# Optimization experiments

Hardware: AMD Instinct MI355X
Metric: run time of the kernel (lower is better)

Reference implementation:

```python
import jax, jax.numpy as jnp
import numpy as np
import math

DIM = 1024
DIM_HEAD = 64
HEADS = 16
HIDDEN = DIM_HEAD * HEADS
EPS = 1e-5


def layer_norm(x, g, b):
    m = jnp.mean(x, axis=-1, keepdims=True)
    v = jnp.var(x, axis=-1, keepdims=True)
    return (x - m) * jax.lax.rsqrt(v + EPS) * g + b


def setup_inputs() -> dict:
    key = jax.random.key(0)
    ks = jax.random.split(key, 8)
    B, n, n_l = 8, 4096, 64
    x = jax.random.normal(ks[0], (B, n, DIM), dtype=jnp.float32)
    latents = jax.random.normal(ks[1], (B, n_l, DIM), dtype=jnp.float32)
    # LayerNorm params
    g_media = jnp.ones((DIM,), jnp.float32)
    b_media = jnp.zeros((DIM,), jnp.float32)
    g_lat = jnp.ones((DIM,), jnp.float32)
    b_lat = jnp.zeros((DIM,), jnp.float32)
    # Linear weights stored as [in, out] so y = x @ W (no bias, as in source)
    s = 1.0 / math.sqrt(DIM)
    Wq = jax.random.uniform(ks[2], (DIM, HIDDEN), jnp.float32, -s, s)
    Wkv = jax.random.uniform(ks[3], (DIM, 2 * HIDDEN), jnp.float32, -s, s)
    so = 1.0 / math.sqrt(HIDDEN)
    Wout = jax.random.uniform(ks[4], (HIDDEN, DIM), jnp.float32, -so, so)
    return {"x": x, "latents": latents, "g_media": g_media, "b_media": b_media,
            "g_lat": g_lat, "b_lat": b_lat, "Wq": Wq, "Wkv": Wkv, "Wout": Wout}


def reference(x, latents, g_media, b_media, g_lat, b_lat, Wq, Wkv, Wout):
    B, n, _ = x.shape
    n_l = latents.shape[1]
    scale = math.sqrt(DIM_HEAD)

    xn = layer_norm(x, g_media, b_media)          # [B, n, D]
    ln_ = layer_norm(latents, g_lat, b_lat)       # [B, n_l, D]

    ctx = jnp.concatenate([xn, ln_], axis=1)      # [B, n+n_l, D]

    q = (ln_ @ Wq).reshape(B, n_l, HEADS, DIM_HEAD).transpose(0, 2, 1, 3)
    kv = ctx @ Wkv                                 # [B, n+n_l, 2*HIDDEN]
    k, v = jnp.split(kv, 2, axis=-1)
    k = k.reshape(B, n + n_l, HEADS, DIM_HEAD).transpose(0, 2, 1, 3)
    v = v.reshape(B, n + n_l, HEADS, DIM_HEAD).transpose(0, 2, 1, 3)

    # scores: [B, H, n_l, n+n_l]; note: no pre-softmax scaling (faithful to source)
    scores = jnp.einsum('bhqd,bhkd->bhqk', q, k)
    scores = scores - jax.lax.stop_gradient(jnp.max(scores, axis=-1, keepdims=True))
    attn = jax.nn.softmax(scores, axis=-1) / scale  # post-softmax scale (faithful)

    out = jnp.einsum('bhqk,bhkd->bhqd', attn, v)   # [B, H, n_l, d]
    out = out.transpose(0, 2, 1, 3).reshape(B, n_l, HIDDEN)
    return out @ Wout                               # [B, n_l, D]
```

## Files before the change

kernel.cpp:

```cpp
#include <hip/hip_runtime.h>

typedef unsigned short u16;
typedef unsigned int u32;
typedef __attribute__((ext_vector_type(8))) short bf16x8;
typedef __attribute__((ext_vector_type(4))) float f32x4;

#define BB   8
#define SN   4096
#define NLQ  64
#define SS   4160
#define DD   1024
#define HH   16
#define DHD  64
#define KV2  2048
#define BNL  512

__device__ __forceinline__ u16 f2bf(float f){
  unsigned int u = __float_as_uint(f);
  u = (u + 0x7fffu + ((u >> 16) & 1u)) >> 16;
  return (u16)u;
}

__device__ __forceinline__ void stc(float* p, float v){ *p = v; }
__device__ __forceinline__ void stc(u16* p, float v){ *p = f2bf(v); }

__device__ __forceinline__ void async_copy16(const u16* g, u16* l){
  __builtin_amdgcn_global_load_lds(
      (const __attribute__((address_space(1))) unsigned int*)g,
      (__attribute__((address_space(3))) unsigned int*)l,
      16, 0, 0);
}

__global__ __launch_bounds__(256) void ln_kernel(
    const float* __restrict__ x, const float* __restrict__ lat,
    const float* __restrict__ g_m, const float* __restrict__ b_m,
    const float* __restrict__ g_l, const float* __restrict__ b_l,
    u16* __restrict__ ctx, u16* __restrict__ latn)
{
  int r = blockIdx.x;
  int b = r / SS, p = r % SS;
  bool isl = (p >= SN);
  const float* src = isl ? lat + ((size_t)b*NLQ + (p-SN))*DD
                         : x   + ((size_t)b*SN + p)*DD;
  const float* gg = isl ? g_l : g_m;
  const float* bb = isl ? b_l : b_m;
  int t = threadIdx.x;
  float4 v = ((const float4*)src)[t];
  float s = v.x + v.y + v.z + v.w;
  float q = v.x*v.x + v.y*v.y + v.z*v.z + v.w*v.w;
  #pragma unroll
  for (int off = 32; off > 0; off >>= 1){
    s += __shfl_down(s, off);
    q += __shfl_down(q, off);
  }
  __shared__ float red[12];
  int lane = t & 63, wid = t >> 6;
  if (lane == 0){ red[wid] = s; red[4+wid] = q; }
  __syncthreads();
  if (t == 0){
    float ts = red[0]+red[1]+red[2]+red[3];
    float tq = red[4]+red[5]+red[6]+red[7];
    float mean = ts * (1.0f/DD);
    float var  = tq * (1.0f/DD) - mean*mean;
    red[8] = mean;
    red[9] = rsqrtf(var + 1e-5f);
  }
  __syncthreads();
  float mean = red[8], rs = red[9];
  float4 gv = ((const float4*)gg)[t];
  float4 bv = ((const float4*)bb)[t];
  ushort4 o;
  o.x = f2bf((v.x-mean)*rs*gv.x + bv.x);
  o.y = f2bf((v.y-mean)*rs*gv.y + bv.y);
  o.z = f2bf((v.z-mean)*rs*gv.z + bv.z);
  o.w = f2bf((v.w-mean)*rs*gv.w + bv.w);
  ((ushort4*)ctx)[(size_t)r*(DD/4) + t] = o;
  if (isl) ((ushort4*)latn)[((size_t)b*NLQ + (p-SN))*(DD/4) + t] = o;
}

__global__ void tcast(const float* __restrict__ in, u16* __restrict__ out,
                      int R, int C)
{
  __shared__ float tile[32][33];
  int c0 = blockIdx.x*32, r0 = blockIdx.y*32;
  int tx = threadIdx.x, ty = threadIdx.y;
  #pragma unroll
  for (int j = 0; j < 4; j++)
    tile[ty + j*8][tx] = in[(size_t)(r0 + ty + j*8)*C + c0 + tx];
  __syncthreads();
  #pragma unroll
  for (int j = 0; j < 4; j++)
    out[(size_t)(c0 + ty + j*8)*R + r0 + tx] = f2bf(tile[tx][ty + j*8]);
}

__global__ void vtrans(const u16* __restrict__ kv, u16* __restrict__ vT)
{
  __shared__ u16 tile[32][33];
  int bl = blockIdx.z;
  int s0 = blockIdx.x*32, c0 = blockIdx.y*32;
  int tx = threadIdx.x, ty = threadIdx.y;
  const u16* in = kv + (size_t)bl*SS*KV2 + DD;
  u16* outp = vT + (size_t)bl*DD*SS;
  #pragma unroll
  for (int j = 0; j < 4; j++)
    tile[ty + j*8][tx] = in[(size_t)(s0 + ty + j*8)*KV2 + c0 + tx];
  __syncthreads();
  #pragma unroll
  for (int j = 0; j < 4; j++)
    outp[(size_t)(c0 + ty + j*8)*SS + s0 + tx] = tile[tx][ty + j*8];
}

__global__ __launch_bounds__(256) void attn_fused(
    const u16* __restrict__ qg,
    const u16* __restrict__ kvg,
    const u16* __restrict__ vTg,
    u16* __restrict__ aog)
{
  __shared__ __align__(16) char smem[70144];
  u16* Kt   = (u16*)smem;
  u16* Vt   = (u16*)(smem + 32768);
  u16* Qt   = (u16*)(smem + 65536);
  float* wsum = (float*)(smem + 69632);
  float* Osum = (float*)smem;

  int z = blockIdx.z;
  int bl = z / HH, h = z % HH;
  int qh = blockIdx.x;
  const u16* qp = qg  + (size_t)(bl*NLQ + qh*32)*DD + h*DHD;
  const u16* kp = kvg + (size_t)bl*SS*KV2 + h*DHD;
  const u16* vp = vTg + (size_t)bl*DD*SS + (size_t)h*DHD*SS;
  u16*       op = aog + (size_t)(bl*NLQ + qh*32)*DD + h*DHD;

  int tid = threadIdx.x;
  int w = tid >> 6, lane = tid & 63, quad = lane >> 4, l16 = lane & 15;
  int r8 = lane >> 3, c8 = lane & 7;
  int r4 = lane >> 4, c16 = lane & 15;

  async_copy16(qp + (size_t)(w*8 + r8)*DD + (c8 ^ r8)*8, &Qt[(w*8)*64]);
  #pragma unroll
  for (int j = 0; j < 4; j++){
    int row = w*32 + j*8 + r8;
    async_copy16(kp + (size_t)row*KV2 + ((c8 ^ (row&7))*8), &Kt[(w*32+j*8)*64]);
  }
  #pragma unroll
  for (int j = 0; j < 4; j++){
    int row = w*16 + j*4 + r4;
    async_copy16(vp + (size_t)row*SS + ((c16 ^ (row&7))*8), &Vt[(w*16+j*4)*128]);
  }
  __syncthreads();

  bf16x8 qf[2][2];
  #pragma unroll
  for (int nb = 0; nb < 2; nb++)
    #pragma unroll
    for (int kc = 0; kc < 2; kc++){
      int qrow = nb*16 + l16;
      qf[nb][kc] = *(const bf16x8*)&Qt[qrow*64 + (((kc*4+quad) ^ (qrow&7))*8)];
    }

  int addrP[2];
  addrP[0] = (((quad&1)*2 + 0)*16 + l16)*4;
  addrP[1] = (((quad&1)*2 + 1)*16 + l16)*4;
  bool hiq = (quad >= 2);

  f32x4 acc[4][2] = {};
  float ssum[2] = {0.f, 0.f};

  for (int it = 0; it <= 32; it++){
    int cur = it & 1, nxt = cur ^ 1;
    u16* Ktc = Kt + cur*(128*64);
    u16* Vtc = Vt + cur*(64*128);

    if (it < 32){
      int kb = (it+1)*128;
      u16* Ktn = Kt + nxt*(128*64);
      u16* Vtn = Vt + nxt*(64*128);
      #pragma unroll
      for (int j = 0; j < 4; j++){
        int row = w*32 + j*8 + r8;
        int key = kb + row; if (key > SS-1) key = SS-1;
        async_copy16(kp + (size_t)key*KV2 + ((c8 ^ (row&7))*8), &Ktn[(w*32+j*8)*64]);
      }
      #pragma unroll
      for (int j = 0; j < 4; j++){
        int row = w*16 + j*4 + r4;
        int s0i = kb + ((c16 ^ (row&7))*8); if (s0i > SS-8) s0i = SS-8;
        async_copy16(vp + (size_t)row*SS + s0i, &Vtn[(w*16+j*4)*128]);
      }
    }

    if (it < 32 || w < 2){
      bf16x8 kf[2][2];
      #pragma unroll
      for (int kb2 = 0; kb2 < 2; kb2++)
        #pragma unroll
        for (int kc = 0; kc < 2; kc++){
          int krow = w*32 + kb2*16 + l16;
          kf[kb2][kc] = *(const bf16x8*)&Ktc[krow*64 + (((kc*4+quad) ^ (krow&7))*8)];
        }
      f32x4 s[2][2] = {};
      #pragma unroll
      for (int kc = 0; kc < 2; kc++)
        #pragma unroll
        for (int kb2 = 0; kb2 < 2; kb2++)
          #pragma unroll
          for (int nb = 0; nb < 2; nb++)
            s[kb2][nb] = __builtin_amdgcn_mfma_f32_16x16x32_bf16(
                kf[kb2][kc], qf[nb][kc], s[kb2][nb], 0, 0, 0);

      #pragma unroll
      for (int kb2 = 0; kb2 < 2; kb2++)
        #pragma unroll
        for (int nb = 0; nb < 2; nb++)
          #pragma unroll
          for (int r = 0; r < 4; r++){
            float e = __expf(s[kb2][nb][r]);
            s[kb2][nb][r] = e;
            ssum[nb] += e;
          }

      u32 pk[2][2][2];
      #pragma unroll
      for (int nb = 0; nb < 2; nb++)
        #pragma unroll
        for (int kb2 = 0; kb2 < 2; kb2++)
          #pragma unroll
          for (int t = 0; t < 2; t++)
            pk[nb][kb2][t] = ((u32)f2bf(s[kb2][nb][2*t+1]) << 16)
                           |  (u32)f2bf(s[kb2][nb][2*t]);
      int4 pbv[2];
      #pragma unroll
      for (int nb = 0; nb < 2; nb++)
        #pragma unroll
        for (int j2 = 0; j2 < 4; j2++){
          int a = addrP[j2>>1];
          int t0 = __builtin_amdgcn_ds_bpermute(a, (int)pk[nb][0][j2&1]);
          int t1 = __builtin_amdgcn_ds_bpermute(a, (int)pk[nb][1][j2&1]);
          ((int*)&pbv[nb])[j2] = hiq ? t1 : t0;
        }

      #pragma unroll
      for (int mb = 0; mb < 4; mb++){
        int vrow = mb*16 + l16;
        bf16x8 vf = *(const bf16x8*)&Vtc[vrow*128 + (((w*4+quad) ^ (vrow&7))*8)];
        #pragma unroll
        for (int nb = 0; nb < 2; nb++)
          acc[mb][nb] = __builtin_amdgcn_mfma_f32_16x16x32_bf16(
              vf, *(const bf16x8*)&pbv[nb], acc[mb][nb], 0, 0, 0);
      }
    }
    __syncthreads();
  }

  #pragma unroll
  for (int nb = 0; nb < 2; nb++){
    float v = ssum[nb];
    v += __shfl_xor(v, 16);
    v += __shfl_xor(v, 32);
    ssum[nb] = v;
  }
  if (quad == 0){
    wsum[w*32 + l16]      = ssum[0];
    wsum[w*32 + 16 + l16] = ssum[1];
  }
  float* Ow = Osum + w*(64*33);
  #pragma unroll
  for (int mb = 0; mb < 4; mb++)
    #pragma unroll
    for (int nb = 0; nb < 2; nb++)
      #pragma unroll
      for (int r = 0; r < 4; r++)
        Ow[(mb*16 + quad*4 + r)*33 + nb*16 + l16] = acc[mb][nb][r];
  __syncthreads();

  int q = tid >> 3, d0 = (tid & 7)*8;
  float l = wsum[q] + wsum[32+q] + wsum[64+q] + wsum[96+q];
  float inv = 1.0f / (l * 8.0f);
  u16 ov[8];
  #pragma unroll
  for (int j = 0; j < 8; j++){
    float sv = Osum[0*2112 + (d0+j)*33 + q] + Osum[1*2112 + (d0+j)*33 + q]
             + Osum[2*2112 + (d0+j)*33 + q] + Osum[3*2112 + (d0+j)*33 + q];
    ov[j] = f2bf(sv * inv);
  }
  *(int4*)&op[(size_t)q*DD + d0] = *(int4*)ov;
}

template<typename OutT>
__global__ __launch_bounds__(256) void gemm_bt(
    const u16* __restrict__ A0, long aSB, long aSH, int lda, int M,
    const u16* __restrict__ B0, long bSB, long bSH, int ldb, int N,
    OutT* __restrict__ C0, long cSB, long cSH, int ldc,
    int K, int zH)
{
  int z = blockIdx.z;
  int bl = z / zH, h = z % zH;
  const u16* A = A0 + (size_t)bl*aSB + (size_t)h*aSH;
  const u16* B = B0 + (size_t)bl*bSB + (size_t)h*bSH;
  OutT* C = C0 + (size_t)bl*cSB + (size_t)h*cSH;
  int row0 = blockIdx.x * 128, col0 = blockIdx.y * 128;

  __shared__ u16 As[128*64];
  __shared__ u16 Bs[128*64];

  int tid = threadIdx.x;
  int lane = tid & 63, w = tid >> 6;
  int wr = w >> 1, wc = w & 1;
  int quad = lane >> 4, l16 = lane & 15;
  int r8 = lane >> 3, c8 = lane & 7;

  f32x4 acc[4][4] = {};

  const u16* apg[4]; const u16* bpg[4];
  u16* asl[4]; u16* bsl[4];
  #pragma unroll
  for (int j = 0; j < 4; j++){
    int rl = w*32 + j*8 + r8;
    int ra = row0 + rl; if (ra > M-1) ra = M-1;
    int rb = col0 + rl; if (rb > N-1) rb = N-1;
    apg[j] = A + (size_t)ra*lda + (c8 ^ r8)*8;
    bpg[j] = B + (size_t)rb*ldb + (c8 ^ r8)*8;
    asl[j] = &As[(w*32 + j*8)*64];
    bsl[j] = &Bs[(w*32 + j*8)*64];
  }

  for (int k0 = 0; k0 < K; k0 += 64){
    #pragma unroll
    for (int j = 0; j < 4; j++){
      async_copy16(apg[j], asl[j]);
      async_copy16(bpg[j], bsl[j]);
      apg[j] += 64; bpg[j] += 64;
    }
    __syncthreads();
    #pragma unroll
    for (int kc = 0; kc < 2; kc++){
      bf16x8 af[4], bfv[4];
      #pragma unroll
      for (int mi = 0; mi < 4; mi++){
        int rowa = wr*64 + mi*16 + l16;
        af[mi] = *(const bf16x8*)&As[rowa*64 + (((kc*4+quad) ^ (l16&7))*8)];
      }
      #pragma unroll
      for (int ni = 0; ni < 4; ni++){
        int rowb = wc*64 + ni*16 + l16;
        bfv[ni] = *(const bf16x8*)&Bs[rowb*64 + (((kc*4+quad) ^ (l16&7))*8)];
      }
      #pragma unroll
      for (int mi = 0; mi < 4; mi++)
        #pragma unroll
        for (int ni = 0; ni < 4; ni++)
          acc[mi][ni] = __builtin_amdgcn_mfma_f32_16x16x32_bf16(
              af[mi], bfv[ni], acc[mi][ni], 0, 0, 0);
    }
    __syncthreads();
  }

  #pragma unroll
  for (int mi = 0; mi < 4; mi++){
    int grow_base = row0 + wr*64 + mi*16 + quad*4;
    #pragma unroll
    for (int ni = 0; ni < 4; ni++){
      int gcol = col0 + wc*64 + ni*16 + l16;
      if (gcol < N){
        #pragma unroll
        for (int r2 = 0; r2 < 4; r2++){
          int grow = grow_base + r2;
          if (grow < M) stc(C + (size_t)grow*ldc + gcol, acc[mi][ni][r2]);
        }
      }
    }
  }
}

extern "C" void kernel_launch(void* const* d_in, const int* in_sizes, int n_in,
                              void* d_out, int out_size, void* d_ws, size_t ws_size,
                              hipStream_t stream)
{
  const float* x    = (const float*)d_in[0];
  const float* lat  = (const float*)d_in[1];
  const float* g_m  = (const float*)d_in[2];
  const float* b_m  = (const float*)d_in[3];
  const float* g_l  = (const float*)d_in[4];
  const float* b_l  = (const float*)d_in[5];
  const float* Wq   = (const float*)d_in[6];
  const float* Wkv  = (const float*)d_in[7];
  const float* Wout = (const float*)d_in[8];
  float* out = (float*)d_out;

  char* wp = (char*)d_ws;
  size_t off = 0;
  auto carve = [&](size_t bytes)->char*{
    char* p = wp + off; off += (bytes + 255) & ~(size_t)255; return p;
  };
  u16* ctx   = (u16*)carve((size_t)BB*SS*DD*2);
  u16* latn  = (u16*)carve((size_t)BNL*DD*2);
  u16* WqT   = (u16*)carve((size_t)DD*DD*2);
  u16* WkvT  = (u16*)carve((size_t)KV2*DD*2);
  u16* WoutT = (u16*)carve((size_t)DD*DD*2);
  u16* qb    = (u16*)carve((size_t)BNL*DD*2);
  u16* ao    = (u16*)carve((size_t)BNL*DD*2);
  size_t fixed = off;

  auto need = [&](int n)->size_t{
    size_t t = fixed;
    t += (((size_t)n*SS*KV2*2 + 255) & ~(size_t)255);
    t += (((size_t)n*DD*SS*2  + 255) & ~(size_t)255);
    t += 4096;
    return t;
  };
  int nb = 1;
  if      (need(8) <= ws_size) nb = 8;
  else if (need(4) <= ws_size) nb = 4;
  else if (need(2) <= ws_size) nb = 2;

  u16* kv = (u16*)carve((size_t)nb*SS*KV2*2);
  u16* vT = (u16*)carve((size_t)nb*DD*SS*2);

  dim3 tb(32, 8);
  tcast<<<dim3(DD/32,  DD/32), tb, 0, stream>>>(Wq,   WqT,   DD, DD);
  tcast<<<dim3(KV2/32, DD/32), tb, 0, stream>>>(Wkv,  WkvT,  DD, KV2);
  tcast<<<dim3(DD/32,  DD/32), tb, 0, stream>>>(Wout, WoutT, DD, DD);

  ln_kernel<<<BB*SS, 256, 0, stream>>>(x, lat, g_m, b_m, g_l, b_l, ctx, latn);

  gemm_bt<u16><<<dim3(BNL/128, DD/128, 1), 256, 0, stream>>>(
      latn, 0, 0, DD, BNL,
      WqT,  0, 0, DD, DD,
      qb,   0, 0, DD, DD, 1);

  int ng = BB / nb;
  for (int g = 0; g < ng; g++){
    int Mkv = nb * SS;
    gemm_bt<u16><<<dim3((Mkv+127)/128, KV2/128, 1), 256, 0, stream>>>(
        ctx + (size_t)g*nb*SS*DD, 0, 0, DD, Mkv,
        WkvT, 0, 0, DD, KV2,
        kv,   0, 0, KV2, DD, 1);

    vtrans<<<dim3(SS/32, DD/32, nb), tb, 0, stream>>>(kv, vT);

    attn_fused<<<dim3(2, 1, nb*HH), 256, 0, stream>>>(
        qb + (size_t)g*nb*NLQ*DD, kv, vT, ao + (size_t)g*nb*NLQ*DD);
  }

  gemm_bt<float><<<dim3(BNL/128, DD/128, 1), 256, 0, stream>>>(
      ao,    0, 0, DD, BNL,
      WoutT, 0, 0, DD, DD,
      out,   0, 0, DD, DD, 1);
}
```

Before: 535.6 us.

## Fuse V transpose into KV projection GEMM epilogue with split K/V outputs

Replaces the generic KV GEMM plus separate vtrans kernel with a dedicated gemm_kv whose epilogue writes K row-major and writes V already transposed, staged through swizzled shared memory. This removes one kernel launch and the full write-then-read-back of the V half of kv, which was read again and written again as vT. The attention kernel now reads K with stride DD and V with a runtime stride ldv. The new GEMM is single-buffered and its V epilogue adds an extra LDS pass and barrier.

Measured after the change: 513.9 us. 1.04x faster.

```diff
diff --git a/kernel.cpp b/kernel.cpp
--- a/kernel.cpp
+++ b/kernel.cpp
@@ -93,27 +93,11 @@
     out[(size_t)(c0 + ty + j*8)*R + r0 + tx] = f2bf(tile[tx][ty + j*8]);
 }
 
-__global__ void vtrans(const u16* __restrict__ kv, u16* __restrict__ vT)
-{
-  __shared__ u16 tile[32][33];
-  int bl = blockIdx.z;
-  int s0 = blockIdx.x*32, c0 = blockIdx.y*32;
-  int tx = threadIdx.x, ty = threadIdx.y;
-  const u16* in = kv + (size_t)bl*SS*KV2 + DD;
-  u16* outp = vT + (size_t)bl*DD*SS;
-  #pragma unroll
-  for (int j = 0; j < 4; j++)
-    tile[ty + j*8][tx] = in[(size_t)(s0 + ty + j*8)*KV2 + c0 + tx];
-  __syncthreads();
-  #pragma unroll
-  for (int j = 0; j < 4; j++)
-    outp[(size_t)(c0 + ty + j*8)*SS + s0 + tx] = tile[tx][ty + j*8];
-}
-
 __global__ __launch_bounds__(256) void attn_fused(
     const u16* __restrict__ qg,
-    const u16* __restrict__ kvg,
+    const u16* __restrict__ kkg,
     const u16* __restrict__ vTg,
+    int ldv,
     u16* __restrict__ aog)
 {
   __shared__ __align__(16) char smem[70144];
@@ -127,8 +111,8 @@
   int bl = z / HH, h = z % HH;
   int qh = blockIdx.x;
   const u16* qp = qg  + (size_t)(bl*NLQ + qh*32)*DD + h*DHD;
-  const u16* kp = kvg + (size_t)bl*SS*KV2 + h*DHD;
-  const u16* vp = vTg + (size_t)bl*DD*SS + (size_t)h*DHD*SS;
+  const u16* kp = kkg + (size_t)bl*SS*DD + h*DHD;
+  const u16* vp = vTg + (size_t)(h*DHD)*ldv + (size_t)bl*SS;
   u16*       op = aog + (size_t)(bl*NLQ + qh*32)*DD + h*DHD;
 
   int tid = threadIdx.x;
@@ -140,12 +124,12 @@
   #pragma unroll
   for (int j = 0; j < 4; j++){
     int row = w*32 + j*8 + r8;
-    async_copy16(kp + (size_t)row*KV2 + ((c8 ^ (row&7))*8), &Kt[(w*32+j*8)*64]);
+    async_copy16(kp + (size_t)row*DD + ((c8 ^ (row&7))*8), &Kt[(w*32+j*8)*64]);
   }
   #pragma unroll
   for (int j = 0; j < 4; j++){
     int row = w*16 + j*4 + r4;
-    async_copy16(vp + (size_t)row*SS + ((c16 ^ (row&7))*8), &Vt[(w*16+j*4)*128]);
+    async_copy16(vp + (size_t)row*ldv + ((c16 ^ (row&7))*8), &Vt[(w*16+j*4)*128]);
   }
   __syncthreads();
 
@@ -179,13 +163,13 @@
       for (int j = 0; j < 4; j++){
         int row = w*32 + j*8 + r8;
         int key = kb + row; if (key > SS-1) key = SS-1;
-        async_copy16(kp + (size_t)key*KV2 + ((c8 ^ (row&7))*8), &Ktn[(w*32+j*8)*64]);
+        async_copy16(kp + (size_t)key*DD + ((c8 ^ (row&7))*8), &Ktn[(w*32+j*8)*64]);
       }
       #pragma unroll
       for (int j = 0; j < 4; j++){
         int row = w*16 + j*4 + r4;
         int s0i = kb + ((c16 ^ (row&7))*8); if (s0i > SS-8) s0i = SS-8;
-        async_copy16(vp + (size_t)row*SS + s0i, &Vtn[(w*16+j*4)*128]);
+        async_copy16(vp + (size_t)row*ldv + s0i, &Vtn[(w*16+j*4)*128]);
       }
     }
 
@@ -284,6 +268,115 @@
     ov[j] = f2bf(sv * inv);
   }
   *(int4*)&op[(size_t)q*DD + d0] = *(int4*)ov;
+}
+
+__global__ __launch_bounds__(256) void gemm_kv(
+    const u16* __restrict__ A, int M,
+    const u16* __restrict__ B,
+    u16* __restrict__ kk,
+    u16* __restrict__ vt, int ldv)
+{
+  int row0 = blockIdx.x * 128, col0 = blockIdx.y * 128;
+
+  __shared__ u16 smem_all[2*128*64];
+  u16* As = smem_all;
+  u16* Bs = smem_all + 128*64;
+
+  int tid = threadIdx.x;
+  int lane = tid & 63, w = tid >> 6;
+  int wr = w >> 1, wc = w & 1;
+  int quad = lane >> 4, l16 = lane & 15;
+  int r8 = lane >> 3, c8 = lane & 7;
+
+  f32x4 acc[4][4] = {};
+
+  const u16* apg[4]; const u16* bpg[4];
+  u16* asl[4]; u16* bsl[4];
+  #pragma unroll
+  for (int j = 0; j < 4; j++){
+    int rl = w*32 + j*8 + r8;
+    int ra = row0 + rl; if (ra > M-1) ra = M-1;
+    int rb = col0 + rl;
+    apg[j] = A + (size_t)ra*DD + (c8 ^ r8)*8;
+    bpg[j] = B + (size_t)rb*DD + (c8 ^ r8)*8;
+    asl[j] = &As[(w*32 + j*8)*64];
+    bsl[j] = &Bs[(w*32 + j*8)*64];
+  }
+
+  for (int k0 = 0; k0 < DD; k0 += 64){
+    #pragma unroll
+    for (int j = 0; j < 4; j++){
+      async_copy16(apg[j], asl[j]);
+      async_copy16(bpg[j], bsl[j]);
+      apg[j] += 64; bpg[j] += 64;
+    }
+    __syncthreads();
+    #pragma unroll
+    for (int kc = 0; kc < 2; kc++){
+      bf16x8 af[4], bfv[4];
+      #pragma unroll
+      for (int mi = 0; mi < 4; mi++){
+        int rowa = wr*64 + mi*16 + l16;
+        af[mi] = *(const bf16x8*)&As[rowa*64 + (((kc*4+quad) ^ (l16&7))*8)];
+      }
+      #pragma unroll
+      for (int ni = 0; ni < 4; ni++){
+        int rowb = wc*64 + ni*16 + l16;
+        bfv[ni] = *(const bf16x8*)&Bs[rowb*64 + (((kc*4+quad) ^ (l16&7))*8)];
+      }
+      #pragma unroll
+      for (int mi = 0; mi < 4; mi++)
+        #pragma unroll
+        for (int ni = 0; ni < 4; ni++)
+          acc[mi][ni] = __builtin_amdgcn_mfma_f32_16x16x32_bf16(
+              af[mi], bfv[ni], acc[mi][ni], 0, 0, 0);
+    }
+    __syncthreads();
+  }
+
+  if (col0 < DD){
+    #pragma unroll
+    for (int mi = 0; mi < 4; mi++){
+      int grow_base = row0 + wr*64 + mi*16 + quad*4;
+      #pragma unroll
+      for (int ni = 0; ni < 4; ni++){
+        int gcol = col0 + wc*64 + ni*16 + l16;
+        #pragma unroll
+        for (int r2 = 0; r2 < 4; r2++){
+          int grow = grow_base + r2;
+          if (grow < M) kk[(size_t)grow*DD + gcol] = f2bf(acc[mi][ni][r2]);
+        }
+      }
+    }
+  } else {
+    u16* Tt = smem_all;
+    #pragma unroll
+    for (int mi = 0; mi < 4; mi++){
+      int c = wr*16 + mi*4 + quad;
+      #pragma unroll
+      for (int ni = 0; ni < 4; ni++){
+        int dl = wc*64 + ni*16 + l16;
+        int cs = c ^ (dl & 31);
+        u16 tmp[4];
+        #pragma unroll
+        for (int r2 = 0; r2 < 4; r2++) tmp[r2] = f2bf(acc[mi][ni][r2]);
+        *(uint2*)&Tt[dl*128 + cs*4] = *(const uint2*)tmp;
+      }
+    }
+    __syncthreads();
+    int d0 = col0 - DD;
+    #pragma unroll
+    for (int p = 0; p < 16; p++){
+      int gi = p*256 + tid;
+      int d = gi >> 5, c = gi & 31;
+      int cs = c ^ (d & 31);
+      int grow = row0 + c*4;
+      if (grow < M){
+        uint2 val = *(const uint2*)&Tt[d*128 + cs*4];
+        *(uint2*)&vt[(size_t)(d0 + d)*ldv + grow] = val;
+      }
+    }
+  }
 }
 
 template<typename OutT>
@@ -403,8 +496,8 @@
 
   auto need = [&](int n)->size_t{
     size_t t = fixed;
-    t += (((size_t)n*SS*KV2*2 + 255) & ~(size_t)255);
-    t += (((size_t)n*DD*SS*2  + 255) & ~(size_t)255);
+    t += (((size_t)n*SS*DD*2 + 255) & ~(size_t)255);
+    t += (((size_t)DD*n*SS*2 + 255) & ~(size_t)255);
     t += 4096;
     return t;
   };
@@ -413,8 +506,8 @@
   else if (need(4) <= ws_size) nb = 4;
   else if (need(2) <= ws_size) nb = 2;
 
-  u16* kv = (u16*)carve((size_t)nb*SS*KV2*2);
-  u16* vT = (u16*)carve((size_t)nb*DD*SS*2);
+  u16* kk  = (u16*)carve((size_t)nb*SS*DD*2);
+  u16* vT2 = (u16*)carve((size_t)DD*nb*SS*2);
 
   dim3 tb(32, 8);
   tcast<<<dim3(DD/32,  DD/32), tb, 0, stream>>>(Wq,   WqT,   DD, DD);
@@ -431,15 +524,11 @@
   int ng = BB / nb;
   for (int g = 0; g < ng; g++){
     int Mkv = nb * SS;
-    gemm_bt<u16><<<dim3((Mkv+127)/128, KV2/128, 1), 256, 0, stream>>>(
-        ctx + (size_t)g*nb*SS*DD, 0, 0, DD, Mkv,
-        WkvT, 0, 0, DD, KV2,
-        kv,   0, 0, KV2, DD, 1);
-
-    vtrans<<<dim3(SS/32, DD/32, nb), tb, 0, stream>>>(kv, vT);
+    gemm_kv<<<dim3((Mkv+127)/128, KV2/128, 1), 256, 0, stream>>>(
+        ctx + (size_t)g*nb*SS*DD, Mkv, WkvT, kk, vT2, Mkv);
 
     attn_fused<<<dim3(2, 1, nb*HH), 256, 0, stream>>>(
-        qb + (size_t)g*nb*NLQ*DD, kv, vT, ao + (size_t)g*nb*NLQ*DD);
+        qb + (size_t)g*nb*NLQ*DD, kk, vT2, Mkv, ao + (size_t)g*nb*NLQ*DD);
   }
 
   gemm_bt<float><<<dim3(BNL/128, DD/128, 1), 256, 0, stream>>>(
```
